# Kernel optimization log

Measured on AMD Instinct MI355X. Metric: run time of the kernel, lower is better.

## Reference

```python
import jax, jax.numpy as jnp
import numpy as np

B, S, D = 2, 4096, 2048
H = 16
DN, DR = 128, 64          # qk_nope_head_dim, qk_rope_head_dim
DQK = DN + DR             # 192
DV = 128                  # v_head_dim
QL, KVL = 512, 512        # q_lora_rank, kv_lora_rank
L = 64                    # block_len
SCALE = DQK ** -0.5
ROPE_THETA = 10000.0


def rms_norm(x, w, eps=1e-6):
    x = x.astype(jnp.float32)
    return x * jax.lax.rsqrt(jnp.mean(x * x, axis=-1, keepdims=True) + eps) * w


def apply_rope(x, cos, sin):
    # x: [b, s, h, d]; cos/sin: [s, d//2]; pairs are consecutive (view(-1,2))
    shp = x.shape
    x2 = x.reshape(shp[:-1] + (-1, 2))
    xr, xi = x2[..., 0], x2[..., 1]
    c = cos[None, :, None, :]
    s_ = sin[None, :, None, :]
    yr = xr * c - xi * s_
    yi = xr * s_ + xi * c
    return jnp.stack([yr, yi], axis=-1).reshape(shp)


def ssa(q, k, v, init_state):
    # chunked causal linear attention; q,k: [b,s,h,dk], v: [b,s,h,dv]
    b, s, h, dk = q.shape
    dv = v.shape[-1]
    nc = s // L
    qc = q.reshape(b, nc, L, h, dk)
    kc = k.reshape(b, nc, L, h, dk)
    vc = v.reshape(b, nc, L, h, dv)
    # per-chunk k^T v outer products -> [b,c,h,dk,dv]
    kv = jnp.einsum('bclhk,bclhv->bchkv', kc, vc)
    cs = jnp.cumsum(kv, axis=1)
    # exclusive prefix (state at chunk start) + initial state
    states = jnp.concatenate([jnp.zeros_like(cs[:, :1]), cs[:, :-1]], axis=1) + init_state[:, None]
    inter = jnp.einsum('bclhk,bchkv->bclhv', qc, states)
    sc = jnp.einsum('bclhk,bcmhk->bchlm', qc, kc)
    mask = jnp.tril(jnp.ones((L, L), dtype=bool))
    sc = jnp.where(mask, sc, 0.0)
    intra = jnp.einsum('bchlm,bcmhv->bclhv', sc, vc)
    return (inter + intra).reshape(b, s, h, dv)


def setup_inputs() -> dict:
    key = jax.random.key(0)
    ks = jax.random.split(key, 8)
    x = jax.random.normal(ks[0], (B, S, D), dtype=jnp.float32)
    # rope tables for qk_rope_head_dim
    inv = 1.0 / (ROPE_THETA ** (np.arange(0, DR, 2, dtype=np.float32) / DR))
    ang = np.outer(np.arange(S, dtype=np.float32), inv)
    cos = jnp.asarray(np.cos(ang), dtype=jnp.float32)
    sin = jnp.asarray(np.sin(ang), dtype=jnp.float32)
    std = 0.02
    wq_a = jax.random.normal(ks[1], (QL, D), dtype=jnp.float32) * std
    wq_b = jax.random.normal(ks[2], (H * DQK, QL), dtype=jnp.float32) * std
    wkv_a = jax.random.normal(ks[3], (KVL + DR, D), dtype=jnp.float32) * std
    wkv_b = jax.random.normal(ks[4], (H * (DN + DV), KVL), dtype=jnp.float32) * std
    wo = jax.random.normal(ks[5], (D, H * DV), dtype=jnp.float32) * std
    q_norm_w = jnp.ones((QL,), dtype=jnp.float32)
    kv_norm_w = jnp.ones((KVL,), dtype=jnp.float32)
    init_state = jnp.zeros((B, H, DQK, DV), dtype=jnp.float32)
    return {"x": x, "start_pos": 0, "cos": cos, "sin": sin,
            "wq_a": wq_a, "wq_b": wq_b, "wkv_a": wkv_a, "wkv_b": wkv_b,
            "wo": wo, "q_norm_w": q_norm_w, "kv_norm_w": kv_norm_w,
            "init_state": init_state}


def reference(x, start_pos, cos, sin, wq_a, wq_b, wkv_a, wkv_b, wo,
              q_norm_w, kv_norm_w, init_state):
    b, s, _ = x.shape
    q = rms_norm(x @ wq_a.T, q_norm_w) @ wq_b.T
    q = q.reshape(b, s, H, DQK)
    q_nope, q_pe = q[..., :DN], q[..., DN:]
    q_pe = apply_rope(q_pe, cos, sin)
    kvp = x @ wkv_a.T
    kv_lat, k_pe = kvp[..., :KVL], kvp[..., KVL:]
    k_pe = apply_rope(k_pe[:, :, None, :], cos, sin)  # [b,s,1,DR]
    kv = rms_norm(kv_lat, kv_norm_w) @ wkv_b.T
    kv = kv.reshape(b, s, H, DN + DV)
    k_nope, v = kv[..., :DN], kv[..., DN:]
    q = jnp.concatenate([q_nope, q_pe], axis=-1)
    k = jnp.concatenate([k_nope, jnp.broadcast_to(k_pe, (b, s, H, DR))], axis=-1)
    q = jax.nn.elu(q) + 1.0
    k = jax.nn.elu(k) + 1.0
    out = ssa(q, k, v, init_state) * SCALE
    out = out.reshape(b, s, H * DV) @ wo.T
    return out
```

## Files before the change

kernel.cpp:

```cpp
#include <hip/hip_runtime.h>

static __device__ __align__(256) unsigned char g_ws[645200000];

typedef __attribute__((ext_vector_type(8))) __bf16 bf16x8;
typedef __attribute__((ext_vector_type(4))) float  f32x4;
typedef __attribute__((ext_vector_type(8))) unsigned short u16x8;

__device__ __forceinline__ short f2bf(float f) {
    union { float f; unsigned u; } v; v.f = f;
    unsigned r = v.u + 0x7FFFu + ((v.u >> 16) & 1u);
    return (short)(r >> 16);
}
__device__ __forceinline__ float bf2f(unsigned short u) {
    union { unsigned u; float f; } v; v.u = ((unsigned)u) << 16;
    return v.f;
}
__device__ __forceinline__ float elu1(float x) {
    return x > 0.f ? x + 1.f : __expf(x);
}
__device__ __forceinline__ void gload_lds16(const void* g, void* l) {
    __builtin_amdgcn_global_load_lds(
        (const __attribute__((address_space(1))) unsigned int*)g,
        (__attribute__((address_space(3))) unsigned int*)l, 16, 0, 0);
}

#define MFMA16(a, b, c) __builtin_amdgcn_mfma_f32_16x16x32_bf16((a), (b), (c), 0, 0, 0)

__global__ __launch_bounds__(256) void cvt_bf16(
    const float* __restrict__ src, short* __restrict__ dst, int n)
{
    const int i = (blockIdx.x * 256 + threadIdx.x) * 4;
    if (i < n) {
        const float4 v = *(const float4*)(src + i);
        ushort4 o;
        o.x = (unsigned short)f2bf(v.x);
        o.y = (unsigned short)f2bf(v.y);
        o.z = (unsigned short)f2bf(v.z);
        o.w = (unsigned short)f2bf(v.w);
        *(ushort4*)(dst + i) = o;
    }
}

template <int EPI>
__global__ __launch_bounds__(512, 1) void gemm_bn(
    const short* __restrict__ A, int lda,
    const short* __restrict__ Bt, int ldb,
    void* __restrict__ C0, void* __restrict__ C1, int ldc,
    int Nvalid, int K, int nby,
    const float* __restrict__ cosT, const float* __restrict__ sinT)
{
    __shared__ char lds[147456];
    const int t = threadIdx.x;
    const int lane = t & 63, w = t >> 6;

    const int cpx = gridDim.x >> 3;
    const int id = ((int)blockIdx.x & 7) * cpx + ((int)blockIdx.x >> 3);
    const int col0 = (id % nby) * 128;
    const int row0 = (id / nby) * 256;

    const int r8 = lane >> 3;
    const int srcb = ((lane & 7) ^ r8) << 4;
    const char* aSrc = (const char*)A + ((size_t)(row0 + w * 32 + r8) * lda) * 2 + srcb;
    const char* bSrc = (const char*)Bt + ((size_t)(col0 + w * 16 + r8) * ldb) * 2 + srcb;
    const size_t aRow8 = (size_t)lda * 16;
    const size_t bRow8 = (size_t)ldb * 16;
    char* aD = lds + w * 4096 + lane * 16;
    char* bD = lds + 98304 + w * 2048 + lane * 16;

    const int wr = (w >> 1) * 64, wc = (w & 1) * 64;
    const int l15 = lane & 15;
    const int g16 = (lane >> 4) * 16;
    const int rxor = (l15 & 7) << 4;

    const int NT = K >> 6;

    auto STAGE = [&](int j) {
        const int sl = j % 3;
        const size_t kb = (size_t)j * 128;
#pragma unroll
        for (int p = 0; p < 4; ++p)
            gload_lds16(aSrc + kb + p * aRow8, aD + sl * 32768 + p * 1024);
#pragma unroll
        for (int p = 0; p < 2; ++p)
            gload_lds16(bSrc + kb + p * bRow8, bD + sl * 16384 + p * 1024);
    };

    f32x4 acc[4][4];
#pragma unroll
    for (int i = 0; i < 4; ++i)
#pragma unroll
        for (int j = 0; j < 4; ++j) acc[i][j] = (f32x4){0.f, 0.f, 0.f, 0.f};

    STAGE(0); STAGE(1);

#pragma unroll 1
    for (int kt = 0; kt < NT; ++kt) {
        if (kt + 1 < NT) asm volatile("s_waitcnt vmcnt(6)" ::: "memory");
        else             asm volatile("s_waitcnt vmcnt(0)" ::: "memory");
        __builtin_amdgcn_sched_barrier(0);
        __builtin_amdgcn_s_barrier();
        if (kt + 2 < NT) STAGE(kt + 2);
        const char* aS = lds + (kt % 3) * 32768;
        const char* bS = lds + 98304 + (kt % 3) * 16384;
#pragma unroll
        for (int half = 0; half < 2; ++half) {
            const int ko = half * 64;
            bf16x8 af[4], bf4[4];
#pragma unroll
            for (int i = 0; i < 4; ++i)
                af[i] = *(const bf16x8*)(aS + (wr + i * 16 + l15) * 128 + ((ko + g16) ^ rxor));
#pragma unroll
            for (int j = 0; j < 4; ++j)
                bf4[j] = *(const bf16x8*)(bS + (wc + j * 16 + l15) * 128 + ((ko + g16) ^ rxor));
            __builtin_amdgcn_s_setprio(1);
#pragma unroll
            for (int i = 0; i < 4; ++i)
#pragma unroll
                for (int j = 0; j < 4; ++j)
                    acc[i][j] = MFMA16(af[i], bf4[j], acc[i][j]);
            __builtin_amdgcn_s_setprio(0);
        }
    }

    const int rbase = (lane >> 4) * 4;
#pragma unroll
    for (int i = 0; i < 4; ++i)
#pragma unroll
        for (int j = 0; j < 4; ++j) {
            const int cc = col0 + wc + j * 16 + l15;
            if (EPI <= 1) {
                if (cc < Nvalid) {
#pragma unroll
                    for (int q = 0; q < 4; ++q) {
                        const size_t o = (size_t)(row0 + wr + i * 16 + rbase + q) * ldc + cc;
                        if (EPI == 1) ((short*)C0)[o] = f2bf(acc[i][j][q]);
                        else          ((float*)C0)[o] = acc[i][j][q];
                    }
                }
            } else if (EPI == 2) {
                const int hh = cc / 192, d = cc - hh * 192;
#pragma unroll
                for (int q = 0; q < 4; ++q) {
                    const int row = row0 + wr + i * 16 + rbase + q;
                    const int s = row & 4095, b = row >> 12;
                    const float v = acc[i][j][q];
                    const float pv = __shfl_xor(v, 1, 64);
                    float val;
                    if (d >= 128) {
                        const int p = (d - 128) >> 1;
                        const float c = cosT[(size_t)s * 32 + p];
                        const float si = sinT[(size_t)s * 32 + p];
                        val = ((d & 1) == 0) ? (v * c - pv * si) : (pv * si + v * c);
                    } else val = v;
                    ((short*)C0)[((size_t)(b * 16 + hh) * 4096 + s) * 192 + d] = f2bf(elu1(val));
                }
            } else {
                const int hh = cc >> 8, d = cc & 255;
#pragma unroll
                for (int q = 0; q < 4; ++q) {
                    const int row = row0 + wr + i * 16 + rbase + q;
                    const int s = row & 4095, b = row >> 12;
                    const float v = acc[i][j][q];
                    if (d < 128)
                        ((short*)C0)[((size_t)(b * 16 + hh) * 4096 + s) * 192 + d] = f2bf(elu1(v));
                    else
                        ((short*)C1)[((size_t)(b * 16 + hh) * 4096 + s) * 128 + d - 128] = f2bf(v);
                }
            }
        }
}

__global__ __launch_bounds__(256) void rms_rope(
    const short* __restrict__ Y1,
    const float* __restrict__ qw, const float* __restrict__ kvw,
    const float* __restrict__ cosT, const float* __restrict__ sinT,
    short* __restrict__ qn, short* __restrict__ kvn, short* __restrict__ kpe)
{
    __shared__ float red[256];
    const int row = blockIdx.x;
    const int s = row & 4095;
    const int t = threadIdx.x;
    const unsigned short* yr = (const unsigned short*)(Y1 + (size_t)row * 1088);

    float v0 = bf2f(yr[t]), v1 = bf2f(yr[t + 256]);
    red[t] = v0 * v0 + v1 * v1;
    __syncthreads();
    for (int off = 128; off > 0; off >>= 1) {
        if (t < off) red[t] += red[t + off];
        __syncthreads();
    }
    float rs = rsqrtf(red[0] / 512.f + 1e-6f);
    __syncthreads();
    qn[(size_t)row * 512 + t]       = f2bf(v0 * rs * qw[t]);
    qn[(size_t)row * 512 + t + 256] = f2bf(v1 * rs * qw[t + 256]);

    float u0 = bf2f(yr[512 + t]), u1 = bf2f(yr[768 + t]);
    red[t] = u0 * u0 + u1 * u1;
    __syncthreads();
    for (int off = 128; off > 0; off >>= 1) {
        if (t < off) red[t] += red[t + off];
        __syncthreads();
    }
    float rs2 = rsqrtf(red[0] / 512.f + 1e-6f);
    kvn[(size_t)row * 512 + t]       = f2bf(u0 * rs2 * kvw[t]);
    kvn[(size_t)row * 512 + t + 256] = f2bf(u1 * rs2 * kvw[t + 256]);

    if (t < 32) {
        float xr = bf2f(yr[1024 + 2 * t]), xi = bf2f(yr[1024 + 2 * t + 1]);
        float cc = cosT[(size_t)s * 32 + t], sn = sinT[(size_t)s * 32 + t];
        kpe[(size_t)row * 64 + 2 * t]     = f2bf(elu1(xr * cc - xi * sn));
        kpe[(size_t)row * 64 + 2 * t + 1] = f2bf(elu1(xr * sn + xi * cc));
    }
}

__global__ __launch_bounds__(256) void build_kpe(
    const short* __restrict__ kpe, short* __restrict__ k_ssa)
{
    const int row = blockIdx.x;
    const int s = row & 4095, b = row >> 12;
    const int t = threadIdx.x;
    const short* pe = kpe + (size_t)row * 64;
#pragma unroll
    for (int it = 0; it < 4; ++it) {
        const int idx = t + it * 256;
        const int h = idx >> 6, dd = idx & 63;
        k_ssa[((size_t)(b * 16 + h) * 4096 + s) * 192 + 128 + dd] = pe[dd];
    }
}

__global__ __launch_bounds__(256) void init_t_kern(
    const float* __restrict__ init, float* __restrict__ initT)
{
    __shared__ float tile[32][33];
    const int bh = blockIdx.y;
    const int tk = blockIdx.x % 6, tv = blockIdx.x / 6;
    const int r0 = threadIdx.x >> 5, c = threadIdx.x & 31;
    const float* src = init + (size_t)bh * 24576;
    float* dst = initT + (size_t)bh * 24576;
#pragma unroll
    for (int p = 0; p < 4; ++p) {
        const int rr = r0 + 8 * p;
        tile[rr][c] = src[(size_t)(tk * 32 + rr) * 128 + tv * 32 + c];
    }
    __syncthreads();
#pragma unroll
    for (int p = 0; p < 4; ++p) {
        const int rr = r0 + 8 * p;
        dst[(size_t)(tv * 32 + rr) * 192 + tk * 32 + c] = tile[c][rr];
    }
}

__global__ __launch_bounds__(256, 3) void ssa_kv(
    const short* __restrict__ k_ssa, const short* __restrict__ v_ssa,
    short* __restrict__ kvcT)
{
    __shared__ short smem[25600];
    short (*lkt)[72] = (short(*)[72])smem;
    short (*lvt)[72] = (short(*)[72])(smem + 192 * 72);
    short (*outT)[200] = (short(*)[200])smem;
    const int c = blockIdx.x, h = blockIdx.y, b = blockIdx.z;
    const int bh = b * 16 + h;
    const short* Kc = k_ssa + ((size_t)bh * 4096 + c * 64) * 192;
    const short* Vc = v_ssa + ((size_t)bh * 4096 + c * 64) * 128;
    const int t = threadIdx.x, lane = t & 63, w = t >> 6;
    const int l15 = lane & 15, kg = (lane >> 4) * 8, rbase = (lane >> 4) * 4;

    for (int i = t; i < 64 * 48; i += 256) {
        const int row = i / 48, c4 = (i % 48) * 4;
        ushort4 kv4 = *(const ushort4*)(Kc + (size_t)row * 192 + c4);
        lkt[c4 + 0][row] = (short)kv4.x;
        lkt[c4 + 1][row] = (short)kv4.y;
        lkt[c4 + 2][row] = (short)kv4.z;
        lkt[c4 + 3][row] = (short)kv4.w;
    }
    for (int i = t; i < 64 * 32; i += 256) {
        const int row = i >> 5, c4 = (i & 31) * 4;
        ushort4 vv = *(const ushort4*)(Vc + (size_t)row * 128 + c4);
        lvt[c4 + 0][row] = (short)vv.x;
        lvt[c4 + 1][row] = (short)vv.y;
        lvt[c4 + 2][row] = (short)vv.z;
        lvt[c4 + 3][row] = (short)vv.w;
    }
    __syncthreads();

    f32x4 acc[2][12];
#pragma unroll
    for (int i = 0; i < 2; ++i)
#pragma unroll
        for (int j = 0; j < 12; ++j) acc[i][j] = (f32x4){0.f, 0.f, 0.f, 0.f};
#pragma unroll
    for (int ks = 0; ks < 2; ++ks) {
        bf16x8 af[2];
#pragma unroll
        for (int i = 0; i < 2; ++i) af[i] = *(const bf16x8*)&lvt[w * 32 + i * 16 + l15][ks * 32 + kg];
#pragma unroll
        for (int j = 0; j < 12; ++j) {
            const bf16x8 bk = *(const bf16x8*)&lkt[j * 16 + l15][ks * 32 + kg];
#pragma unroll
            for (int i = 0; i < 2; ++i) acc[i][j] = MFMA16(af[i], bk, acc[i][j]);
        }
    }
    __syncthreads();
#pragma unroll
    for (int i = 0; i < 2; ++i)
#pragma unroll
        for (int j = 0; j < 12; ++j)
#pragma unroll
            for (int q = 0; q < 4; ++q)
                outT[w * 32 + i * 16 + rbase + q][j * 16 + l15] = f2bf(acc[i][j][q]);
    __syncthreads();

    short* kvp = kvcT + ((size_t)bh * 64 + c) * 24576;
    for (int i = t; i < 3072; i += 256) {
        const int s8 = i * 8;
        const int row = s8 / 192, col = s8 % 192;
        *(u16x8*)(kvp + s8) = *(const u16x8*)&outT[row][col];
    }
}

__global__ __launch_bounds__(256) void ssa_scan(
    short* __restrict__ kvc, const float* __restrict__ initT)
{
    const int bh = blockIdx.y;
    const int e8 = (blockIdx.x * 256 + threadIdx.x) * 8;
    float st[8];
    {
        const float4 i0 = *(const float4*)(initT + (size_t)bh * 24576 + e8);
        const float4 i1 = *(const float4*)(initT + (size_t)bh * 24576 + e8 + 4);
        st[0] = i0.x; st[1] = i0.y; st[2] = i0.z; st[3] = i0.w;
        st[4] = i1.x; st[5] = i1.y; st[6] = i1.z; st[7] = i1.w;
    }
    short* p = kvc + (size_t)bh * 64 * 24576 + e8;
    for (int cc = 0; cc < 64; ++cc) {
        const u16x8 v = *(const u16x8*)p;
        u16x8 o;
#pragma unroll
        for (int j = 0; j < 8; ++j) o[j] = (unsigned short)f2bf(st[j]);
        *(u16x8*)p = o;
#pragma unroll
        for (int j = 0; j < 8; ++j) st[j] += bf2f(v[j]);
        p += 24576;
    }
}

__global__ __launch_bounds__(256, 2) void ssa_out(
    const short* __restrict__ q_ssa, const short* __restrict__ k_ssa,
    const short* __restrict__ v_ssa, const short* __restrict__ states,
    short* __restrict__ attnb)
{
    __shared__ short lk[64][200];
    __shared__ short lvt[128][72];
    __shared__ short lst[128][104];
    __shared__ short lsc[64][72];
    const int c = blockIdx.x, h = blockIdx.y, b = blockIdx.z;
    const int bh = b * 16 + h;
    const short* Qb = q_ssa + ((size_t)bh * 4096 + c * 64) * 192;
    const short* Kc = k_ssa + ((size_t)bh * 4096 + c * 64) * 192;
    const short* Vc = v_ssa + ((size_t)bh * 4096 + c * 64) * 128;
    const short* st = states + ((size_t)bh * 64 + c) * 24576;
    const int t = threadIdx.x, lane = t & 63, w = t >> 6;
    const int l15 = lane & 15, kg = (lane >> 4) * 8, rbase = (lane >> 4) * 4;

    bf16x8 aq[6];
    {
        const short* Qr = Qb + (size_t)(w * 16 + l15) * 192 + kg;
#pragma unroll
        for (int ks = 0; ks < 6; ++ks) aq[ks] = *(const bf16x8*)(Qr + ks * 32);
    }
    for (int i = t; i < 1536; i += 256) {
        const int row = i / 24, c8 = (i % 24) * 8;
        *(u16x8*)&lk[row][c8] = *(const u16x8*)(Kc + (size_t)row * 192 + c8);
    }
    for (int i = t; i < 2048; i += 256) {
        const int row = i >> 5, c4 = (i & 31) * 4;
        ushort4 vv = *(const ushort4*)(Vc + (size_t)row * 128 + c4);
        lvt[c4 + 0][row] = (short)vv.x;
        lvt[c4 + 1][row] = (short)vv.y;
        lvt[c4 + 2][row] = (short)vv.z;
        lvt[c4 + 3][row] = (short)vv.w;
    }
    for (int i = t; i < 1536; i += 256) {
        const int row = i / 12, c8 = (i % 12) * 8;
        *(u16x8*)&lst[row][c8] = *(const u16x8*)(st + (size_t)row * 192 + c8);
    }
    __syncthreads();

    {
        f32x4 sc[4];
#pragma unroll
        for (int j = 0; j < 4; ++j) sc[j] = (f32x4){0.f, 0.f, 0.f, 0.f};
#pragma unroll
        for (int ks = 0; ks < 6; ++ks)
#pragma unroll
            for (int j = 0; j < 4; ++j) {
                const bf16x8 bk = *(const bf16x8*)&lk[j * 16 + l15][ks * 32 + kg];
                sc[j] = MFMA16(aq[ks], bk, sc[j]);
            }
#pragma unroll
        for (int j = 0; j < 4; ++j)
#pragma unroll
            for (int q = 0; q < 4; ++q) {
                const int l = w * 16 + rbase + q;
                const int m = j * 16 + l15;
                lsc[l][m] = f2bf((m <= l) ? sc[j][q] : 0.f);
            }
    }
    __syncthreads();

    f32x4 acc[8];
#pragma unroll
    for (int j = 0; j < 8; ++j) acc[j] = (f32x4){0.f, 0.f, 0.f, 0.f};
#pragma unroll
    for (int ks = 0; ks < 2; ++ks) {
        const bf16x8 as = *(const bf16x8*)&lsc[w * 16 + l15][ks * 32 + kg];
#pragma unroll
        for (int j = 0; j < 8; ++j) {
            const bf16x8 bv = *(const bf16x8*)&lvt[j * 16 + l15][ks * 32 + kg];
            acc[j] = MFMA16(as, bv, acc[j]);
        }
    }
#pragma unroll
    for (int ks = 0; ks < 3; ++ks)
#pragma unroll
        for (int j = 0; j < 8; ++j) {
            const bf16x8 bs = *(const bf16x8*)&lst[j * 16 + l15][ks * 32 + kg];
            acc[j] = MFMA16(aq[ks], bs, acc[j]);
        }
    __syncthreads();
    for (int i = t; i < 1536; i += 256) {
        const int row = i / 12, c8 = (i % 12) * 8;
        *(u16x8*)&lst[row][c8] = *(const u16x8*)(st + (size_t)row * 192 + 96 + c8);
    }
    __syncthreads();
#pragma unroll
    for (int ks = 3; ks < 6; ++ks)
#pragma unroll
        for (int j = 0; j < 8; ++j) {
            const bf16x8 bs = *(const bf16x8*)&lst[j * 16 + l15][(ks - 3) * 32 + kg];
            acc[j] = MFMA16(aq[ks], bs, acc[j]);
        }

    const float scale = 0.07216878364870322f;
#pragma unroll
    for (int j = 0; j < 8; ++j)
#pragma unroll
        for (int q = 0; q < 4; ++q) {
            const int l = w * 16 + rbase + q;
            const int dv = j * 16 + l15;
            attnb[((size_t)(b * 4096 + c * 64 + l)) * 2048 + h * 128 + dv] = f2bf(acc[j][q] * scale);
        }
}

extern "C" void kernel_launch(void* const* d_in, const int* in_sizes, int n_in,
                              void* d_out, int out_size, void* d_ws, size_t ws_size,
                              hipStream_t stream) {
    const float* x     = (const float*)d_in[0];
    const float* cosT  = (const float*)d_in[2];
    const float* sinT  = (const float*)d_in[3];
    const float* wq_a  = (const float*)d_in[4];
    const float* wq_b  = (const float*)d_in[5];
    const float* wkv_a = (const float*)d_in[6];
    const float* wkv_b = (const float*)d_in[7];
    const float* wo    = (const float*)d_in[8];
    const float* qw    = (const float*)d_in[9];
    const float* kvw   = (const float*)d_in[10];
    const float* init  = (const float*)d_in[11];
    float* out = (float*)d_out;

    void* base = nullptr;
    hipGetSymbolAddress(&base, HIP_SYMBOL(g_ws));
    char* ws = (char*)base;
    size_t off = 0;
    auto take = [&](size_t bytes) -> char* {
        char* p = ws + off;
        off += (bytes + 255) & ~(size_t)255;
        return p;
    };
    short* xb    = (short*)take((size_t)8192 * 2048 * 2);
    short* wab   = (short*)take((size_t)1280 * 2048 * 2);
    short* wqbb  = (short*)take((size_t)3072 * 512 * 2);
    short* wkvbb = (short*)take((size_t)4096 * 512 * 2);
    short* wob   = (short*)take((size_t)2048 * 2048 * 2);
    short* y1b   = (short*)take((size_t)8192 * 1088 * 2);
    short* qnb   = (short*)take((size_t)8192 * 512 * 2);
    short* kvnb  = (short*)take((size_t)8192 * 512 * 2);
    short* kpe   = (short*)take((size_t)8192 * 64 * 2);
    short* qs    = (short*)take((size_t)2 * 16 * 4096 * 192 * 2);
    short* ksb   = (short*)take((size_t)2 * 16 * 4096 * 192 * 2);
    short* vsb   = (short*)take((size_t)2 * 16 * 4096 * 128 * 2);
    short* kvcT  = (short*)take((size_t)2048 * 24576 * 2);
    float* initT = (float*)take((size_t)32 * 24576 * 4);
    short* attnb = (short*)take((size_t)8192 * 2048 * 2);

    cvt_bf16<<<(8192 * 2048 / 4 + 255) / 256, 256, 0, stream>>>(x, xb, 8192 * 2048);
    cvt_bf16<<<(512 * 2048 / 4 + 255) / 256, 256, 0, stream>>>(wq_a, wab, 512 * 2048);
    cvt_bf16<<<(576 * 2048 / 4 + 255) / 256, 256, 0, stream>>>(wkv_a, wab + (size_t)512 * 2048, 576 * 2048);
    hipMemsetAsync(wab + (size_t)1088 * 2048, 0, (size_t)192 * 2048 * 2, stream);
    cvt_bf16<<<(3072 * 512 / 4 + 255) / 256, 256, 0, stream>>>(wq_b, wqbb, 3072 * 512);
    cvt_bf16<<<(4096 * 512 / 4 + 255) / 256, 256, 0, stream>>>(wkv_b, wkvbb, 4096 * 512);
    cvt_bf16<<<(2048 * 2048 / 4 + 255) / 256, 256, 0, stream>>>(wo, wob, 2048 * 2048);
    init_t_kern<<<dim3(24, 32), 256, 0, stream>>>(init, initT);

    gemm_bn<1><<<320, 512, 0, stream>>>(xb, 2048, wab, 2048, y1b, nullptr, 1088, 1088, 2048, 10, nullptr, nullptr);
    rms_rope<<<8192, 256, 0, stream>>>(y1b, qw, kvw, cosT, sinT, qnb, kvnb, kpe);
    gemm_bn<2><<<768, 512, 0, stream>>>(qnb, 512, wqbb, 512, qs, nullptr, 0, 3072, 512, 24, cosT, sinT);
    gemm_bn<3><<<1024, 512, 0, stream>>>(kvnb, 512, wkvbb, 512, ksb, vsb, 0, 4096, 512, 32, nullptr, nullptr);
    build_kpe<<<8192, 256, 0, stream>>>(kpe, ksb);
    ssa_kv<<<dim3(64, 16, 2), 256, 0, stream>>>(ksb, vsb, kvcT);
    ssa_scan<<<dim3(12, 32), 256, 0, stream>>>(kvcT, initT);
    ssa_out<<<dim3(64, 16, 2), 256, 0, stream>>>(qs, ksb, vsb, kvcT, attnb);
    gemm_bn<0><<<512, 512, 0, stream>>>(attnb, 2048, wob, 2048, out, nullptr, 2048, 2048, 2048, 16, nullptr, nullptr);
}
```

Before: 648.3 us.

## Use 256x256 GEMM tiles with 4-stage K32 pipeline and tune small kernels

The GEMM tile grows from 256x128 to 256x256, with a 4-deep LDS ring of K=32 slices and a new swizzle, to raise data reuse per loaded byte. rms_rope now does both reductions with wave shuffles and a single barrier. build_kpe switches to 16-byte vector copies. ssa_scan uses more threads with 2 elements each to expose more parallelism. The larger tile doubles accumulator registers and halves the block count, so small GEMMs may underfill the GPU (the first GEMM runs only 160 blocks).

Result: faster. 610.9 us (-5.8%).

```diff
diff --git a/kernel.cpp b/kernel.cpp
--- a/kernel.cpp
+++ b/kernel.cpp
@@ -42,89 +42,84 @@
 }
 
 template <int EPI>
-__global__ __launch_bounds__(512, 1) void gemm_bn(
+__global__ __launch_bounds__(512, 1) void gemm256(
     const short* __restrict__ A, int lda,
     const short* __restrict__ Bt, int ldb,
     void* __restrict__ C0, void* __restrict__ C1, int ldc,
     int Nvalid, int K, int nby,
     const float* __restrict__ cosT, const float* __restrict__ sinT)
 {
-    __shared__ char lds[147456];
+    __shared__ char lds[131072];
     const int t = threadIdx.x;
     const int lane = t & 63, w = t >> 6;
 
     const int cpx = gridDim.x >> 3;
     const int id = ((int)blockIdx.x & 7) * cpx + ((int)blockIdx.x >> 3);
-    const int col0 = (id % nby) * 128;
+    const int col0 = (id % nby) * 256;
     const int row0 = (id / nby) * 256;
 
-    const int r8 = lane >> 3;
-    const int srcb = ((lane & 7) ^ r8) << 4;
-    const char* aSrc = (const char*)A + ((size_t)(row0 + w * 32 + r8) * lda) * 2 + srcb;
-    const char* bSrc = (const char*)Bt + ((size_t)(col0 + w * 16 + r8) * ldb) * 2 + srcb;
-    const size_t aRow8 = (size_t)lda * 16;
-    const size_t bRow8 = (size_t)ldb * 16;
-    char* aD = lds + w * 4096 + lane * 16;
-    char* bD = lds + 98304 + w * 2048 + lane * 16;
-
-    const int wr = (w >> 1) * 64, wc = (w & 1) * 64;
+    const int r_in = lane >> 2;
+    const int srcb = (((lane & 3) ^ ((lane >> 3) & 3)) << 4);
+    const char* aSrc = (const char*)A + ((size_t)(row0 + w * 32 + r_in) * lda) * 2 + srcb;
+    const char* bSrc = (const char*)Bt + ((size_t)(col0 + w * 32 + r_in) * ldb) * 2 + srcb;
+    const size_t aRow16 = (size_t)lda * 32;
+    const size_t bRow16 = (size_t)ldb * 32;
+    char* aD = lds + w * 2048 + lane * 16;
+    char* bD = lds + 65536 + w * 2048 + lane * 16;
+
+    const int wr = (w >> 2) * 128, wc = (w & 3) * 64;
     const int l15 = lane & 15;
-    const int g16 = (lane >> 4) * 16;
-    const int rxor = (l15 & 7) << 4;
-
-    const int NT = K >> 6;
+    const int g16 = (lane >> 4) << 4;
+    const int rxor = ((l15 >> 1) & 3) << 4;
+
+    const int NT = K >> 5;
 
     auto STAGE = [&](int j) {
-        const int sl = j % 3;
-        const size_t kb = (size_t)j * 128;
-#pragma unroll
-        for (int p = 0; p < 4; ++p)
-            gload_lds16(aSrc + kb + p * aRow8, aD + sl * 32768 + p * 1024);
-#pragma unroll
-        for (int p = 0; p < 2; ++p)
-            gload_lds16(bSrc + kb + p * bRow8, bD + sl * 16384 + p * 1024);
+        const int sl = (j & 3) * 16384;
+        const size_t kb = (size_t)j * 64;
+        gload_lds16(aSrc + kb,          aD + sl);
+        gload_lds16(aSrc + kb + aRow16, aD + sl + 1024);
+        gload_lds16(bSrc + kb,          bD + sl);
+        gload_lds16(bSrc + kb + bRow16, bD + sl + 1024);
     };
 
-    f32x4 acc[4][4];
-#pragma unroll
-    for (int i = 0; i < 4; ++i)
+    f32x4 acc[8][4];
+#pragma unroll
+    for (int i = 0; i < 8; ++i)
 #pragma unroll
         for (int j = 0; j < 4; ++j) acc[i][j] = (f32x4){0.f, 0.f, 0.f, 0.f};
 
-    STAGE(0); STAGE(1);
+    STAGE(0); STAGE(1); STAGE(2);
 
 #pragma unroll 1
     for (int kt = 0; kt < NT; ++kt) {
-        if (kt + 1 < NT) asm volatile("s_waitcnt vmcnt(6)" ::: "memory");
-        else             asm volatile("s_waitcnt vmcnt(0)" ::: "memory");
+        if (kt < NT - 2)        asm volatile("s_waitcnt vmcnt(8)" ::: "memory");
+        else if (kt == NT - 2)  asm volatile("s_waitcnt vmcnt(4)" ::: "memory");
+        else                    asm volatile("s_waitcnt vmcnt(0)" ::: "memory");
         __builtin_amdgcn_sched_barrier(0);
         __builtin_amdgcn_s_barrier();
-        if (kt + 2 < NT) STAGE(kt + 2);
-        const char* aS = lds + (kt % 3) * 32768;
-        const char* bS = lds + 98304 + (kt % 3) * 16384;
-#pragma unroll
-        for (int half = 0; half < 2; ++half) {
-            const int ko = half * 64;
-            bf16x8 af[4], bf4[4];
-#pragma unroll
-            for (int i = 0; i < 4; ++i)
-                af[i] = *(const bf16x8*)(aS + (wr + i * 16 + l15) * 128 + ((ko + g16) ^ rxor));
+        if (kt + 3 < NT) STAGE(kt + 3);
+        const char* aS = lds + (kt & 3) * 16384;
+        const char* bS = lds + 65536 + (kt & 3) * 16384;
+        bf16x8 af[8], bf4[4];
+#pragma unroll
+        for (int i = 0; i < 8; ++i)
+            af[i] = *(const bf16x8*)(aS + (wr + i * 16 + l15) * 64 + (g16 ^ rxor));
+#pragma unroll
+        for (int j = 0; j < 4; ++j)
+            bf4[j] = *(const bf16x8*)(bS + (wc + j * 16 + l15) * 64 + (g16 ^ rxor));
+        __builtin_amdgcn_s_setprio(1);
+#pragma unroll
+        for (int i = 0; i < 8; ++i)
 #pragma unroll
             for (int j = 0; j < 4; ++j)
-                bf4[j] = *(const bf16x8*)(bS + (wc + j * 16 + l15) * 128 + ((ko + g16) ^ rxor));
-            __builtin_amdgcn_s_setprio(1);
-#pragma unroll
-            for (int i = 0; i < 4; ++i)
-#pragma unroll
-                for (int j = 0; j < 4; ++j)
-                    acc[i][j] = MFMA16(af[i], bf4[j], acc[i][j]);
-            __builtin_amdgcn_s_setprio(0);
-        }
+                acc[i][j] = MFMA16(af[i], bf4[j], acc[i][j]);
+        __builtin_amdgcn_s_setprio(0);
     }
 
     const int rbase = (lane >> 4) * 4;
 #pragma unroll
-    for (int i = 0; i < 4; ++i)
+    for (int i = 0; i < 8; ++i)
 #pragma unroll
         for (int j = 0; j < 4; ++j) {
             const int cc = col0 + wc + j * 16 + l15;
@@ -176,32 +171,29 @@
     const float* __restrict__ cosT, const float* __restrict__ sinT,
     short* __restrict__ qn, short* __restrict__ kvn, short* __restrict__ kpe)
 {
-    __shared__ float red[256];
+    __shared__ float wsq[4], wsk[4];
     const int row = blockIdx.x;
     const int s = row & 4095;
     const int t = threadIdx.x;
+    const int w = t >> 6, lane = t & 63;
     const unsigned short* yr = (const unsigned short*)(Y1 + (size_t)row * 1088);
 
-    float v0 = bf2f(yr[t]), v1 = bf2f(yr[t + 256]);
-    red[t] = v0 * v0 + v1 * v1;
-    __syncthreads();
-    for (int off = 128; off > 0; off >>= 1) {
-        if (t < off) red[t] += red[t + off];
-        __syncthreads();
-    }
-    float rs = rsqrtf(red[0] / 512.f + 1e-6f);
-    __syncthreads();
-    qn[(size_t)row * 512 + t]       = f2bf(v0 * rs * qw[t]);
-    qn[(size_t)row * 512 + t + 256] = f2bf(v1 * rs * qw[t + 256]);
-
-    float u0 = bf2f(yr[512 + t]), u1 = bf2f(yr[768 + t]);
-    red[t] = u0 * u0 + u1 * u1;
-    __syncthreads();
-    for (int off = 128; off > 0; off >>= 1) {
-        if (t < off) red[t] += red[t + off];
-        __syncthreads();
-    }
-    float rs2 = rsqrtf(red[0] / 512.f + 1e-6f);
+    const float v0 = bf2f(yr[t]),       v1 = bf2f(yr[t + 256]);
+    const float u0 = bf2f(yr[512 + t]), u1 = bf2f(yr[768 + t]);
+    float sq = v0 * v0 + v1 * v1;
+    float sk = u0 * u0 + u1 * u1;
+#pragma unroll
+    for (int off = 32; off > 0; off >>= 1) {
+        sq += __shfl_xor(sq, off, 64);
+        sk += __shfl_xor(sk, off, 64);
+    }
+    if (lane == 0) { wsq[w] = sq; wsk[w] = sk; }
+    __syncthreads();
+    const float rs  = rsqrtf((wsq[0] + wsq[1] + wsq[2] + wsq[3]) / 512.f + 1e-6f);
+    const float rs2 = rsqrtf((wsk[0] + wsk[1] + wsk[2] + wsk[3]) / 512.f + 1e-6f);
+
+    qn[(size_t)row * 512 + t]        = f2bf(v0 * rs * qw[t]);
+    qn[(size_t)row * 512 + t + 256]  = f2bf(v1 * rs * qw[t + 256]);
     kvn[(size_t)row * 512 + t]       = f2bf(u0 * rs2 * kvw[t]);
     kvn[(size_t)row * 512 + t + 256] = f2bf(u1 * rs2 * kvw[t + 256]);
 
@@ -213,19 +205,15 @@
     }
 }
 
-__global__ __launch_bounds__(256) void build_kpe(
+__global__ __launch_bounds__(128) void build_kpe(
     const short* __restrict__ kpe, short* __restrict__ k_ssa)
 {
     const int row = blockIdx.x;
     const int s = row & 4095, b = row >> 12;
     const int t = threadIdx.x;
-    const short* pe = kpe + (size_t)row * 64;
-#pragma unroll
-    for (int it = 0; it < 4; ++it) {
-        const int idx = t + it * 256;
-        const int h = idx >> 6, dd = idx & 63;
-        k_ssa[((size_t)(b * 16 + h) * 4096 + s) * 192 + 128 + dd] = pe[dd];
-    }
+    const int h = t >> 3, d8 = (t & 7) * 8;
+    const u16x8 v = *(const u16x8*)(kpe + (size_t)row * 64 + d8);
+    *(u16x8*)(k_ssa + ((size_t)(b * 16 + h) * 4096 + s) * 192 + 128 + d8) = v;
 }
 
 __global__ __launch_bounds__(256) void init_t_kern(
@@ -322,24 +310,19 @@
     short* __restrict__ kvc, const float* __restrict__ initT)
 {
     const int bh = blockIdx.y;
-    const int e8 = (blockIdx.x * 256 + threadIdx.x) * 8;
-    float st[8];
-    {
-        const float4 i0 = *(const float4*)(initT + (size_t)bh * 24576 + e8);
-        const float4 i1 = *(const float4*)(initT + (size_t)bh * 24576 + e8 + 4);
-        st[0] = i0.x; st[1] = i0.y; st[2] = i0.z; st[3] = i0.w;
-        st[4] = i1.x; st[5] = i1.y; st[6] = i1.z; st[7] = i1.w;
-    }
-    short* p = kvc + (size_t)bh * 64 * 24576 + e8;
+    const int e2 = (blockIdx.x * 256 + threadIdx.x) * 2;
+    const float2 iv = *(const float2*)(initT + (size_t)bh * 24576 + e2);
+    float s0 = iv.x, s1 = iv.y;
+    unsigned* p = (unsigned*)(kvc + (size_t)bh * 64 * 24576 + e2);
+#pragma unroll 2
     for (int cc = 0; cc < 64; ++cc) {
-        const u16x8 v = *(const u16x8*)p;
-        u16x8 o;
-#pragma unroll
-        for (int j = 0; j < 8; ++j) o[j] = (unsigned short)f2bf(st[j]);
-        *(u16x8*)p = o;
-#pragma unroll
-        for (int j = 0; j < 8; ++j) st[j] += bf2f(v[j]);
-        p += 24576;
+        const unsigned v = *p;
+        const unsigned o = (unsigned)(unsigned short)f2bf(s0) |
+                           ((unsigned)(unsigned short)f2bf(s1) << 16);
+        *p = o;
+        s0 += bf2f((unsigned short)(v & 0xffffu));
+        s1 += bf2f((unsigned short)(v >> 16));
+        p += 12288;
     }
 }
 
@@ -501,13 +484,13 @@
     cvt_bf16<<<(2048 * 2048 / 4 + 255) / 256, 256, 0, stream>>>(wo, wob, 2048 * 2048);
     init_t_kern<<<dim3(24, 32), 256, 0, stream>>>(init, initT);
 
-    gemm_bn<1><<<320, 512, 0, stream>>>(xb, 2048, wab, 2048, y1b, nullptr, 1088, 1088, 2048, 10, nullptr, nullptr);
+    gemm256<1><<<160, 512, 0, stream>>>(xb, 2048, wab, 2048, y1b, nullptr, 1088, 1088, 2048, 5, nullptr, nullptr);
     rms_rope<<<8192, 256, 0, stream>>>(y1b, qw, kvw, cosT, sinT, qnb, kvnb, kpe);
-    gemm_bn<2><<<768, 512, 0, stream>>>(qnb, 512, wqbb, 512, qs, nullptr, 0, 3072, 512, 24, cosT, sinT);
-    gemm_bn<3><<<1024, 512, 0, stream>>>(kvnb, 512, wkvbb, 512, ksb, vsb, 0, 4096, 512, 32, nullptr, nullptr);
-    build_kpe<<<8192, 256, 0, stream>>>(kpe, ksb);
+    gemm256<2><<<384, 512, 0, stream>>>(qnb, 512, wqbb, 512, qs, nullptr, 0, 3072, 512, 12, cosT, sinT);
+    gemm256<3><<<512, 512, 0, stream>>>(kvnb, 512, wkvbb, 512, ksb, vsb, 0, 4096, 512, 16, nullptr, nullptr);
+    build_kpe<<<8192, 128, 0, stream>>>(kpe, ksb);
     ssa_kv<<<dim3(64, 16, 2), 256, 0, stream>>>(ksb, vsb, kvcT);
-    ssa_scan<<<dim3(12, 32), 256, 0, stream>>>(kvcT, initT);
+    ssa_scan<<<dim3(48, 32), 256, 0, stream>>>(kvcT, initT);
     ssa_out<<<dim3(64, 16, 2), 256, 0, stream>>>(qs, ksb, vsb, kvcT, attnb);
-    gemm_bn<0><<<512, 512, 0, stream>>>(attnb, 2048, wob, 2048, out, nullptr, 2048, 2048, 2048, 16, nullptr, nullptr);
-}
+    gemm256<0><<<256, 512, 0, stream>>>(attnb, 2048, wob, 2048, out, nullptr, 2048, 2048, 2048, 8, nullptr, nullptr);
+}
```
